# Performance work log

Measured on AMD Instinct MI355X. Metric: run time of the kernel, lower is better.

Reference implementation:

```python
import jax, jax.numpy as jnp
import numpy as np

D_MODEL = 768
N_HEADS = 8
D_K = D_MODEL // N_HEADS
D_FF = 2048
EPS = 1e-5


def _layer_norm(x, gamma, beta):
    mu = jnp.mean(x, axis=-1, keepdims=True)
    var = jnp.mean(jnp.square(x - mu), axis=-1, keepdims=True)
    return (x - mu) * jax.lax.rsqrt(var + EPS) * gamma + beta


def setup_inputs() -> dict:
    key = jax.random.key(0)
    ks = jax.random.split(key, 16)
    s = 1.0 / np.sqrt(D_MODEL)
    sf = 1.0 / np.sqrt(D_FF)
    inp = {
        "x": jax.random.normal(ks[0], (4, 2048, D_MODEL), jnp.float32),
        "Wq": jax.random.uniform(ks[1], (D_MODEL, D_MODEL), jnp.float32, -s, s),
        "bq": jnp.zeros((D_MODEL,), jnp.float32),
        "Wk": jax.random.uniform(ks[2], (D_MODEL, D_MODEL), jnp.float32, -s, s),
        "bk": jnp.zeros((D_MODEL,), jnp.float32),
        "Wv": jax.random.uniform(ks[3], (D_MODEL, D_MODEL), jnp.float32, -s, s),
        "bv": jnp.zeros((D_MODEL,), jnp.float32),
        "Wo": jax.random.uniform(ks[4], (D_MODEL, D_MODEL), jnp.float32, -s, s),
        "bo": jnp.zeros((D_MODEL,), jnp.float32),
        "g1": jnp.ones((D_MODEL,), jnp.float32),
        "be1": jnp.zeros((D_MODEL,), jnp.float32),
        "W1": jax.random.uniform(ks[5], (D_MODEL, D_FF), jnp.float32, -s, s),
        "b1": jnp.zeros((D_FF,), jnp.float32),
        "W2": jax.random.uniform(ks[6], (D_FF, D_MODEL), jnp.float32, -sf, sf),
        "b2": jnp.zeros((D_MODEL,), jnp.float32),
        "g2": jnp.ones((D_MODEL,), jnp.float32),
        "be2": jnp.zeros((D_MODEL,), jnp.float32),
    }
    return inp


def reference(x, Wq, bq, Wk, bk, Wv, bv, Wo, bo, g1, be1, W1, b1, W2, b2, g2, be2):
    B, S, D = x.shape
    residual = x
    # projections, split into heads: [B, H, S, d_k]
    def proj(W, b):
        return (x @ W + b).reshape(B, S, N_HEADS, D_K).transpose(0, 2, 1, 3)
    Q, K, V = proj(Wq, bq), proj(Wk, bk), proj(Wv, bv)
    # explicit (non-fused) attention, as in the original
    scores = jnp.einsum('bhqd,bhkd->bhqk', Q, K) / np.sqrt(D_K)  # [B,H,S,S]
    attn = jax.nn.softmax(scores, axis=-1)
    out = jnp.einsum('bhqk,bhkd->bhqd', attn, V)
    out = out.transpose(0, 2, 1, 3).reshape(B, S, D)
    out = out @ Wo + bo
    x1 = _layer_norm(residual + out, g1, be1)
    ff = jax.nn.relu(x1 @ W1 + b1) @ W2 + b2
    return _layer_norm(x1 + ff, g2, be2)
```

## Files before the change

kernel.cpp:

```cpp
#include <hip/hip_runtime.h>
#include <cstdint>
#include <cstddef>

typedef unsigned short u16;
typedef __bf16 bf16x8 __attribute__((ext_vector_type(8)));
typedef float f32x4 __attribute__((ext_vector_type(4)));
typedef float f32x16 __attribute__((ext_vector_type(16)));

#define BATCH 4
#define SEQ   2048
#define DM    768
#define NH    8
#define DK    96
#define DFF   2048
#define MTOK  8192
#define QKVN  2304
#define LOG2E 1.44269504088896340736f

__device__ __forceinline__ u16 f2bf(float f) {
  union { float f; uint32_t u; } v; v.f = f;
  return (u16)((v.u + 0x7fffu + ((v.u >> 16) & 1u)) >> 16);
}
__device__ __forceinline__ float bf2f(u16 b) {
  union { uint32_t u; float f; } v; v.u = (uint32_t)b << 16;
  return v.f;
}
__device__ __forceinline__ bf16x8 ld8(const u16* p) { return *(const bf16x8*)p; }
__device__ __forceinline__ void async16(const u16* g, u16* l) {
  __builtin_amdgcn_global_load_lds((const __attribute__((address_space(1))) void*)g,
                                   (__attribute__((address_space(3))) void*)l, 16, 0, 0);
}

__global__ __launch_bounds__(256)
void prep(const float* __restrict__ x, u16* __restrict__ xb,
          const float* __restrict__ bq, const float* __restrict__ bk,
          const float* __restrict__ bv, float* __restrict__ bqkv,
          const float* __restrict__ Wq, const float* __restrict__ Wk,
          const float* __restrict__ Wv, const float* __restrict__ Wo,
          const float* __restrict__ W1, const float* __restrict__ W2,
          u16* __restrict__ WT, u16* __restrict__ WoT,
          u16* __restrict__ W1T, u16* __restrict__ W2T) {
  __shared__ float t[32][33];
  const int tid = threadIdx.x;
  int bid = blockIdx.x;

  if (bid < 6144) {
    size_t i = (size_t)bid * 1024 + tid * 4;
    float4 f = *(const float4*)(x + i);
    uint2 o;
    o.x = (unsigned)f2bf(f.x) | ((unsigned)f2bf(f.y) << 16);
    o.y = (unsigned)f2bf(f.z) | ((unsigned)f2bf(f.w) << 16);
    *(uint2*)(xb + i) = o;
    return;
  }
  if (bid < 6153) {
    int i = (bid - 6144) * 256 + tid;
    float v = (i < 768) ? bq[i] : (i < 1536) ? bk[i - 768] : bv[i - 1536];
    bqkv[i] = v;
    return;
  }
  bid -= 6153;
  const float* in; u16* out; int C, R, bx, by;
  if (bid < 576)       { in = Wq; out = WT;                 C = 768;  R = 768;  bx = bid % 24;          by = bid / 24; }
  else if (bid < 1152) { in = Wk; out = WT + 768 * 768;     C = 768;  R = 768;  bx = (bid - 576) % 24;  by = (bid - 576) / 24; }
  else if (bid < 1728) { in = Wv; out = WT + 2 * 768 * 768; C = 768;  R = 768;  bx = (bid - 1152) % 24; by = (bid - 1152) / 24; }
  else if (bid < 2304) { in = Wo; out = WoT;                C = 768;  R = 768;  bx = (bid - 1728) % 24; by = (bid - 1728) / 24; }
  else if (bid < 3840) { in = W1; out = W1T;                C = 2048; R = 768;  bx = (bid - 2304) % 64; by = (bid - 2304) / 64; }
  else                 { in = W2; out = W2T;                C = 768;  R = 2048; bx = (bid - 3840) % 24; by = (bid - 3840) / 24; }
  const int r0 = by * 32, c0 = bx * 32;
  const int tx = tid & 31, ty = tid >> 5;
#pragma unroll
  for (int i = 0; i < 4; i++)
    t[ty + i * 8][tx] = in[(size_t)(r0 + ty + i * 8) * C + c0 + tx];
  __syncthreads();
#pragma unroll
  for (int i = 0; i < 4; i++)
    out[(size_t)(c0 + ty + i * 8) * R + r0 + tx] = f2bf(t[tx][ty + i * 8]);
}

__global__ void transpose_v(const u16* __restrict__ v, u16* __restrict__ vt) {
  __shared__ u16 t[32][33];
  int bh = blockIdx.z, b = bh >> 3, h = bh & 7;
  int s0 = blockIdx.x * 32, d0 = blockIdx.y * 32;
  int tx = threadIdx.x, ty = threadIdx.y;
#pragma unroll
  for (int i = 0; i < 4; i++)
    t[ty + i * 8][tx] = v[(size_t)(b * SEQ + s0 + ty + i * 8) * QKVN + h * DK + d0 + tx];
  __syncthreads();
#pragma unroll
  for (int i = 0; i < 4; i++)
    vt[(size_t)(bh * DK + d0 + ty + i * 8) * SEQ + s0 + tx] = t[tx][ty + i * 8];
}

template <int RESID, int RELU, int OUTBF>
__global__ __launch_bounds__(256, 4)
void gemm_bt(const u16* __restrict__ A, const u16* __restrict__ BT,
             const float* __restrict__ bias, const float* __restrict__ resid,
             float* __restrict__ Cf, u16* __restrict__ Cb, int N, int K) {
  __shared__ __align__(16) u16 lA[128 * 64];
  __shared__ __align__(16) u16 lB[128 * 64];
  const int tid = threadIdx.x;
  const int wave = tid >> 6, lane = tid & 63;
  const int quad = lane >> 4, l16 = lane & 15;
  const int wm = wave >> 1, wn = wave & 1;
  const int q8 = gridDim.x >> 3;
  const int wg = (blockIdx.x & 7) * q8 + (blockIdx.x >> 3);
  const int nbx = N >> 7;
  const int tm = (wg / nbx) * 128, tn = (wg % nbx) * 128;

  f32x4 acc[4][4] = {};

  for (int k0 = 0; k0 < K; k0 += 64) {
    __syncthreads();
#pragma unroll
    for (int i = 0; i < 4; i++) {
      int cbase = (wave * 4 + i) * 64;
      int c = cbase + lane;
      int row = c >> 3;
      int scc = (c & 7) ^ (row & 7);
      async16(A + (size_t)(tm + row) * K + k0 + scc * 8, &lA[cbase * 8]);
      async16(BT + (size_t)(tn + row) * K + k0 + scc * 8, &lB[cbase * 8]);
    }
    __syncthreads();
#pragma unroll
    for (int ks = 0; ks < 2; ks++) {
      bf16x8 af[4], bfr[4];
#pragma unroll
      for (int i = 0; i < 4; i++) {
        int ra = wm * 64 + i * 16 + l16;
        af[i] = ld8(&lA[ra * 64 + (((ks * 4 + quad) ^ (ra & 7)) << 3)]);
        int rb = wn * 64 + i * 16 + l16;
        bfr[i] = ld8(&lB[rb * 64 + (((ks * 4 + quad) ^ (rb & 7)) << 3)]);
      }
#pragma unroll
      for (int i = 0; i < 4; i++)
#pragma unroll
        for (int j = 0; j < 4; j++)
          acc[i][j] = __builtin_amdgcn_mfma_f32_16x16x32_bf16(af[i], bfr[j], acc[i][j], 0, 0, 0);
    }
  }

#pragma unroll
  for (int i = 0; i < 4; i++) {
    const int row0 = tm + wm * 64 + i * 16 + quad * 4;
#pragma unroll
    for (int j = 0; j < 4; j++) {
      const int col = tn + wn * 64 + j * 16 + l16;
      const float bv = bias[col];
#pragma unroll
      for (int r = 0; r < 4; r++) {
        float v = acc[i][j][r] + bv;
        if (RESID) v += resid[(size_t)(row0 + r) * N + col];
        if (RELU) v = fmaxf(v, 0.f);
        if (OUTBF) Cb[(size_t)(row0 + r) * N + col] = f2bf(v);
        else       Cf[(size_t)(row0 + r) * N + col] = v;
      }
    }
  }
}

template <int RESID, int RELU, int OUTBF, int RESBF>
__global__ __launch_bounds__(256, 4)
void gemm_bt64(const u16* __restrict__ A, const u16* __restrict__ BT,
               const float* __restrict__ bias, const float* __restrict__ residf,
               const u16* __restrict__ residb,
               float* __restrict__ Cf, u16* __restrict__ Cb, int N, int K) {
  __shared__ __align__(16) u16 lA[128 * 64];
  __shared__ __align__(16) u16 lB[64 * 64];
  const int tid = threadIdx.x;
  const int wave = tid >> 6, lane = tid & 63;
  const int quad = lane >> 4, l16 = lane & 15;
  const int wm = wave >> 1, wn = wave & 1;
  const int q8 = gridDim.x >> 3;
  const int wg = (blockIdx.x & 7) * q8 + (blockIdx.x >> 3);
  const int nbx = N >> 6;
  const int tm = (wg / nbx) * 128, tn = (wg % nbx) * 64;

  f32x4 acc[4][2] = {};

  for (int k0 = 0; k0 < K; k0 += 64) {
    __syncthreads();
#pragma unroll
    for (int i = 0; i < 4; i++) {
      int cbase = (wave * 4 + i) * 64;
      int c = cbase + lane;
      int row = c >> 3;
      int scc = (c & 7) ^ (row & 7);
      async16(A + (size_t)(tm + row) * K + k0 + scc * 8, &lA[cbase * 8]);
    }
#pragma unroll
    for (int i = 0; i < 2; i++) {
      int cbase = (wave * 2 + i) * 64;
      int c = cbase + lane;
      int row = c >> 3;
      int scc = (c & 7) ^ (row & 7);
      async16(BT + (size_t)(tn + row) * K + k0 + scc * 8, &lB[cbase * 8]);
    }
    __syncthreads();
#pragma unroll
    for (int ks = 0; ks < 2; ks++) {
      bf16x8 af[4], bfr[2];
#pragma unroll
      for (int i = 0; i < 4; i++) {
        int ra = wm * 64 + i * 16 + l16;
        af[i] = ld8(&lA[ra * 64 + (((ks * 4 + quad) ^ (ra & 7)) << 3)]);
      }
#pragma unroll
      for (int j = 0; j < 2; j++) {
        int rb = wn * 32 + j * 16 + l16;
        bfr[j] = ld8(&lB[rb * 64 + (((ks * 4 + quad) ^ (rb & 7)) << 3)]);
      }
#pragma unroll
      for (int i = 0; i < 4; i++)
#pragma unroll
        for (int j = 0; j < 2; j++)
          acc[i][j] = __builtin_amdgcn_mfma_f32_16x16x32_bf16(af[i], bfr[j], acc[i][j], 0, 0, 0);
    }
  }

#pragma unroll
  for (int i = 0; i < 4; i++) {
    const int row0 = tm + wm * 64 + i * 16 + quad * 4;
#pragma unroll
    for (int j = 0; j < 2; j++) {
      const int col = tn + wn * 32 + j * 16 + l16;
      const float bv = bias[col];
#pragma unroll
      for (int r = 0; r < 4; r++) {
        float v = acc[i][j][r] + bv;
        if (RESID) {
          if (RESBF) v += bf2f(residb[(size_t)(row0 + r) * N + col]);
          else       v += residf[(size_t)(row0 + r) * N + col];
        }
        if (RELU) v = fmaxf(v, 0.f);
        if (OUTBF) Cb[(size_t)(row0 + r) * N + col] = f2bf(v);
        else       Cf[(size_t)(row0 + r) * N + col] = v;
      }
    }
  }
}

#define KROW 104
#define VROW 64

#define PACK_SLICE(SC, B, DST)                                                   \
  {                                                                              \
    uint32_t u0, u1, u2, u3;                                                     \
    asm("v_cvt_pk_bf16_f32 %0, %1, %2" : "=v"(u0) : "v"(SC[B+0]), "v"(SC[B+1])); \
    asm("v_cvt_pk_bf16_f32 %0, %1, %2" : "=v"(u1) : "v"(SC[B+2]), "v"(SC[B+3])); \
    asm("v_cvt_pk_bf16_f32 %0, %1, %2" : "=v"(u2) : "v"(SC[B+4]), "v"(SC[B+5])); \
    asm("v_cvt_pk_bf16_f32 %0, %1, %2" : "=v"(u3) : "v"(SC[B+6]), "v"(SC[B+7])); \
    asm("v_permlane32_swap_b32 %0, %1" : "+v"(u2), "+v"(u0));                    \
    asm("v_permlane32_swap_b32 %0, %1" : "+v"(u3), "+v"(u1));                    \
    union { uint32_t w[4]; bf16x8 v; } pu_;                                      \
    pu_.w[0] = u0; pu_.w[1] = u1; pu_.w[2] = u2; pu_.w[3] = u3;                  \
    DST = pu_.v;                                                                 \
  }

__global__ __launch_bounds__(512, 4)
void flash_attn(const u16* __restrict__ qkv, const u16* __restrict__ Vt,
                u16* __restrict__ Ob) {
  __shared__ __align__(16) u16 smem[31744];
  const int tid = threadIdx.x, wave = tid >> 6, lane = tid & 63;
  const int l32 = lane & 31, half = lane >> 5;
  const int qsub = wave >> 1, kodd = wave & 1, pair = wave >> 1;
  const int lin = blockIdx.x;
  const int bh = (lin & 7) * 4 + ((lin >> 3) & 3);
  const int qb = lin >> 5;
  const int b = bh >> 3, h = bh & 7;
  const int q0 = qb * 128 + qsub * 32;
  const u16* Qp = qkv;
  const u16* KpB = qkv + 768 + (size_t)b * SEQ * QKVN + h * DK;
  const u16* VtB = Vt + (size_t)bh * DK * SEQ;
  const float cs = 0.10206207262f * LOG2E;
  const float Ms = 16.0f * cs;

  bf16x8 qf[6];
#pragma unroll
  for (int d = 0; d < 6; d++)
    qf[d] = ld8(Qp + (size_t)(b * SEQ + q0 + l32) * QKVN + h * DK + d * 16 + half * 8);

  f32x16 of[3] = {};
  float lp[4] = {0.f, 0.f, 0.f, 0.f};
  bf16x8 pa[2];

  auto stage = [&](int kt, int kb_, int vb_) {
    u16* kd = smem + kb_ * 6656;
    u16* vd = smem + 13312 + vb_ * 6144;
    {
      int sl = tid;
      int row = sl / 13, s = sl - row * 13;
      int c = s > 11 ? 11 : s;
      async16(KpB + (size_t)(kt + row) * QKVN + c * 8, kd + sl * 8);
    }
    if (tid < 320) {
      int sl = 512 + tid;
      int row = sl / 13, s = sl - row * 13;
      int c = s > 11 ? 11 : s;
      async16(KpB + (size_t)(kt + row) * QKVN + c * 8, kd + sl * 8);
    }
    {
      int s = tid;
      int row = s >> 3, c = (s ^ row) & 7;
      async16(VtB + (size_t)row * SEQ + kt + c * 8, vd + s * 8);
    }
    if (tid < 256) {
      int s = 512 + tid;
      int row = s >> 3, c = (s ^ row) & 7;
      async16(VtB + (size_t)row * SEQ + kt + c * 8, vd + s * 8);
    }
  };

  stage(0, 0, 0);
  int vs = 1;
  int vr = 0;
  const int krow = kodd * 32 + l32;

  for (int t = 0; t < 32; t++) {
    __syncthreads();
    if (t + 1 < 32) stage((t + 1) * 64, (t + 1) & 1, vs);
    vs = (vs == 2) ? 0 : vs + 1;

    const u16* kd = smem + (t & 1) * 6656;
    f32x16 sc = {};
    __builtin_amdgcn_s_setprio(1);
#pragma unroll
    for (int d = 0; d < 6; d++) {
      bf16x8 kb = ld8(&kd[krow * KROW + (d * 2 + half) * 8]);
      sc = __builtin_amdgcn_mfma_f32_32x32x16_bf16(kb, qf[d], sc, 0, 0, 0);
    }

    if (t > 0) {
      const u16* vd = smem + 13312 + vr * 6144;
      vr = (vr == 2) ? 0 : vr + 1;
#pragma unroll
      for (int ks = 0; ks < 2; ks++) {
        int gv = kodd * 4 + ks * 2 + half;
#pragma unroll
        for (int db = 0; db < 3; db++) {
          int vrow = db * 32 + l32;
          bf16x8 va = ld8(&vd[vrow * VROW + ((gv ^ vrow) & 7) * 8]);
          of[db] = __builtin_amdgcn_mfma_f32_32x32x16_bf16(va, pa[ks], of[db], 0, 0, 0);
        }
      }
    }
    __builtin_amdgcn_s_setprio(0);

#pragma unroll
    for (int r = 0; r < 16; r++) {
      float p = __builtin_amdgcn_exp2f(sc[r] * cs - Ms);
      lp[r & 3] += p;
      sc[r] = p;
    }
    PACK_SLICE(sc, 0, pa[0])
    PACK_SLICE(sc, 8, pa[1])
  }

  {
    const u16* vd = smem + 13312 + vr * 6144;
#pragma unroll
    for (int ks = 0; ks < 2; ks++) {
      int gv = kodd * 4 + ks * 2 + half;
#pragma unroll
      for (int db = 0; db < 3; db++) {
        int vrow = db * 32 + l32;
        bf16x8 va = ld8(&vd[vrow * VROW + ((gv ^ vrow) & 7) * 8]);
        of[db] = __builtin_amdgcn_mfma_f32_32x32x16_bf16(va, pa[ks], of[db], 0, 0, 0);
      }
    }
  }

  float l_lane = (lp[0] + lp[1]) + (lp[2] + lp[3]);
  float lw = l_lane + __shfl_xor(l_lane, 32);
  float linv = 0.f;
  float* xf = (float*)smem;
  const int q = q0 + l32;
  u16* Orow = Ob + (size_t)(b * SEQ + q) * DM + h * DK;

  __syncthreads();
  if (kodd) {
    float* dst = xf + (pair * 64 + lane) * 33;
#pragma unroll
    for (int r = 0; r < 16; r++) { dst[r] = of[0][r]; dst[16 + r] = of[1][r]; }
    dst[32] = lw;
  }
  __syncthreads();
  if (!kodd) {
    const float* src = xf + (pair * 64 + lane) * 33;
    linv = 1.f / (lw + src[32]);
#pragma unroll
    for (int db = 0; db < 2; db++)
#pragma unroll
      for (int r = 0; r < 16; r++) {
        int dk = db * 32 + (r & 3) + 8 * (r >> 2) + 4 * half;
        Orow[dk] = f2bf((of[db][r] + src[db * 16 + r]) * linv);
      }
  }
  __syncthreads();
  if (kodd) {
    float* dst = xf + (pair * 64 + lane) * 16;
#pragma unroll
    for (int r = 0; r < 16; r++) dst[r] = of[2][r];
  }
  __syncthreads();
  if (!kodd) {
    const float* src = xf + (pair * 64 + lane) * 16;
#pragma unroll
    for (int r = 0; r < 16; r++) {
      int dk = 64 + (r & 3) + 8 * (r >> 2) + 4 * half;
      Orow[dk] = f2bf((of[2][r] + src[r]) * linv);
    }
  }
}

__global__ __launch_bounds__(256)
void ln_kernel(const float* __restrict__ y, const float* __restrict__ g,
               const float* __restrict__ be, float* __restrict__ outf,
               u16* __restrict__ outb) {
  int row = blockIdx.x, t = threadIdx.x;
  const float* yr = y + (size_t)row * DM;
  float v[3], s = 0.f, s2 = 0.f;
#pragma unroll
  for (int i = 0; i < 3; i++) {
    v[i] = yr[t + i * 256];
    s += v[i];
    s2 += v[i] * v[i];
  }
#pragma unroll
  for (int m = 1; m < 64; m <<= 1) {
    s += __shfl_xor(s, m);
    s2 += __shfl_xor(s2, m);
  }
  __shared__ float red[2][4];
  int w = t >> 6;
  if ((t & 63) == 0) { red[0][w] = s; red[1][w] = s2; }
  __syncthreads();
  s = red[0][0] + red[0][1] + red[0][2] + red[0][3];
  s2 = red[1][0] + red[1][1] + red[1][2] + red[1][3];
  float mu = s * (1.f / DM);
  float var = s2 * (1.f / DM) - mu * mu;
  float rs = rsqrtf(var + 1e-5f);
#pragma unroll
  for (int i = 0; i < 3; i++) {
    int e = t + i * 256;
    float o = (v[i] - mu) * rs * g[e] + be[e];
    if (outf) outf[(size_t)row * DM + e] = o;
    if (outb) outb[(size_t)row * DM + e] = f2bf(o);
  }
}

#define SZ_BF 12582912ull
#define SZ_F  25165824ull
#define O_XB   0ull
#define O_WT   (O_XB + SZ_BF)
#define O_WOT  (O_WT + 3538944ull)
#define O_W1T  (O_WOT + 1179648ull)
#define O_W2T  (O_W1T + 3145728ull)
#define O_QKV  (O_W2T + 3145728ull)
#define O_VT   (O_QKV + 37748736ull)
#define O_Y    (O_VT + SZ_BF)
#define O_X1F  (O_Y + SZ_F)
#define O_BIAS (O_X1F + SZ_F)

extern "C" void kernel_launch(void* const* d_in, const int* in_sizes, int n_in,
                              void* d_out, int out_size, void* d_ws, size_t ws_size,
                              hipStream_t stream) {
  const float* x   = (const float*)d_in[0];
  const float* Wq  = (const float*)d_in[1];
  const float* bq  = (const float*)d_in[2];
  const float* Wk  = (const float*)d_in[3];
  const float* bk  = (const float*)d_in[4];
  const float* Wv  = (const float*)d_in[5];
  const float* bv  = (const float*)d_in[6];
  const float* Wo  = (const float*)d_in[7];
  const float* bo  = (const float*)d_in[8];
  const float* g1  = (const float*)d_in[9];
  const float* be1 = (const float*)d_in[10];
  const float* W1  = (const float*)d_in[11];
  const float* b1  = (const float*)d_in[12];
  const float* W2  = (const float*)d_in[13];
  const float* b2  = (const float*)d_in[14];
  const float* g2  = (const float*)d_in[15];
  const float* be2 = (const float*)d_in[16];
  float* out = (float*)d_out;
  char* ws = (char*)d_ws;

  u16* xb    = (u16*)(ws + O_XB);
  u16* WT    = (u16*)(ws + O_WT);
  u16* WoT   = (u16*)(ws + O_WOT);
  u16* W1T   = (u16*)(ws + O_W1T);
  u16* W2T   = (u16*)(ws + O_W2T);
  u16* qkv   = (u16*)(ws + O_QKV);
  u16* vt    = (u16*)(ws + O_VT);
  float* y   = (float*)(ws + O_Y);
  float* bqkv = (float*)(ws + O_BIAS);
  u16* ao   = xb;
  u16* x1b  = qkv;
  u16* hbuf = qkv + (size_t)MTOK * DM;

  prep<<<11529, 256, 0, stream>>>(x, xb, bq, bk, bv, bqkv,
                                  Wq, Wk, Wv, Wo, W1, W2,
                                  WT, WoT, W1T, W2T);

  gemm_bt<0, 0, 1><<<1152, 256, 0, stream>>>(xb, WT, bqkv, nullptr, nullptr, qkv, QKVN, DM);
  transpose_v<<<dim3(64, 3, 32), dim3(32, 8), 0, stream>>>(qkv + 1536, vt);
  flash_attn<<<512, 512, 0, stream>>>(qkv, vt, ao);
  gemm_bt64<1, 0, 0, 0><<<768, 256, 0, stream>>>(ao, WoT, bo, x, nullptr, y, nullptr, DM, DM);
  ln_kernel<<<8192, 256, 0, stream>>>(y, g1, be1, nullptr, x1b);
  gemm_bt<0, 1, 1><<<1024, 256, 0, stream>>>(x1b, W1T, b1, nullptr, nullptr, hbuf, DFF, DM);
  gemm_bt64<1, 0, 0, 1><<<768, 256, 0, stream>>>(hbuf, W2T, b2, nullptr, x1b, y, nullptr, DM, DFF);
  ln_kernel<<<8192, 256, 0, stream>>>(y, g2, be2, out, nullptr);
}
```

Before: 320.3 us.

## Use 256x128 tiles with 512-thread blocks for QKV and FFN1 GEMMs; double-buffer attention

The QKV and W1 GEMMs move to a new kernel with a 256-row M tile and 8 waves, which halves the block count and reuses each loaded B tile across twice as many rows. The flash-attention kernel drops its triple-buffered V staging for plain double buffering. It adds a second barrier per iteration so the next tile is issued only after the current buffers have been read. This shrinks shared memory per block and drops the min-occupancy launch bound, but the extra sync can reduce the overlap between loads and compute.

```diff
diff --git a/kernel.cpp b/kernel.cpp
--- a/kernel.cpp
+++ b/kernel.cpp
@@ -92,12 +92,12 @@
     vt[(size_t)(bh * DK + d0 + ty + i * 8) * SEQ + s0 + tx] = t[tx][ty + i * 8];
 }
 
-template <int RESID, int RELU, int OUTBF>
-__global__ __launch_bounds__(256, 4)
-void gemm_bt(const u16* __restrict__ A, const u16* __restrict__ BT,
-             const float* __restrict__ bias, const float* __restrict__ resid,
-             float* __restrict__ Cf, u16* __restrict__ Cb, int N, int K) {
-  __shared__ __align__(16) u16 lA[128 * 64];
+template <int RELU>
+__global__ __launch_bounds__(512, 4)
+void gemm_bt256(const u16* __restrict__ A, const u16* __restrict__ BT,
+                const float* __restrict__ bias,
+                u16* __restrict__ Cb, int N, int K) {
+  __shared__ __align__(16) u16 lA[256 * 64];
   __shared__ __align__(16) u16 lB[128 * 64];
   const int tid = threadIdx.x;
   const int wave = tid >> 6, lane = tid & 63;
@@ -106,7 +106,7 @@
   const int q8 = gridDim.x >> 3;
   const int wg = (blockIdx.x & 7) * q8 + (blockIdx.x >> 3);
   const int nbx = N >> 7;
-  const int tm = (wg / nbx) * 128, tn = (wg % nbx) * 128;
+  const int tm = (wg / nbx) * 256, tn = (wg % nbx) * 128;
 
   f32x4 acc[4][4] = {};
 
@@ -114,11 +114,18 @@
     __syncthreads();
 #pragma unroll
     for (int i = 0; i < 4; i++) {
-      int cbase = (wave * 4 + i) * 64;
+      int cbase = i * 512 + wave * 64;
       int c = cbase + lane;
       int row = c >> 3;
       int scc = (c & 7) ^ (row & 7);
       async16(A + (size_t)(tm + row) * K + k0 + scc * 8, &lA[cbase * 8]);
+    }
+#pragma unroll
+    for (int i = 0; i < 2; i++) {
+      int cbase = i * 512 + wave * 64;
+      int c = cbase + lane;
+      int row = c >> 3;
+      int scc = (c & 7) ^ (row & 7);
       async16(BT + (size_t)(tn + row) * K + k0 + scc * 8, &lB[cbase * 8]);
     }
     __syncthreads();
@@ -129,8 +136,11 @@
       for (int i = 0; i < 4; i++) {
         int ra = wm * 64 + i * 16 + l16;
         af[i] = ld8(&lA[ra * 64 + (((ks * 4 + quad) ^ (ra & 7)) << 3)]);
-        int rb = wn * 64 + i * 16 + l16;
-        bfr[i] = ld8(&lB[rb * 64 + (((ks * 4 + quad) ^ (rb & 7)) << 3)]);
+      }
+#pragma unroll
+      for (int j = 0; j < 4; j++) {
+        int rb = wn * 64 + j * 16 + l16;
+        bfr[j] = ld8(&lB[rb * 64 + (((ks * 4 + quad) ^ (rb & 7)) << 3)]);
       }
 #pragma unroll
       for (int i = 0; i < 4; i++)
@@ -150,10 +160,8 @@
 #pragma unroll
       for (int r = 0; r < 4; r++) {
         float v = acc[i][j][r] + bv;
-        if (RESID) v += resid[(size_t)(row0 + r) * N + col];
         if (RELU) v = fmaxf(v, 0.f);
-        if (OUTBF) Cb[(size_t)(row0 + r) * N + col] = f2bf(v);
-        else       Cf[(size_t)(row0 + r) * N + col] = v;
+        Cb[(size_t)(row0 + r) * N + col] = f2bf(v);
       }
     }
   }
@@ -257,10 +265,10 @@
     DST = pu_.v;                                                                 \
   }
 
-__global__ __launch_bounds__(512, 4)
+__global__ __launch_bounds__(512)
 void flash_attn(const u16* __restrict__ qkv, const u16* __restrict__ Vt,
                 u16* __restrict__ Ob) {
-  __shared__ __align__(16) u16 smem[31744];
+  __shared__ __align__(16) u16 smem[25600];
   const int tid = threadIdx.x, wave = tid >> 6, lane = tid & 63;
   const int l32 = lane & 31, half = lane >> 5;
   const int qsub = wave >> 1, kodd = wave & 1, pair = wave >> 1;
@@ -284,9 +292,9 @@
   float lp[4] = {0.f, 0.f, 0.f, 0.f};
   bf16x8 pa[2];
 
-  auto stage = [&](int kt, int kb_, int vb_) {
-    u16* kd = smem + kb_ * 6656;
-    u16* vd = smem + 13312 + vb_ * 6144;
+  auto stage = [&](int kt, int buf) {
+    u16* kd = smem + buf * 6656;
+    u16* vd = smem + 13312 + buf * 6144;
     {
       int sl = tid;
       int row = sl / 13, s = sl - row * 13;
@@ -311,15 +319,11 @@
     }
   };
 
-  stage(0, 0, 0);
-  int vs = 1;
-  int vr = 0;
+  stage(0, 0);
   const int krow = kodd * 32 + l32;
 
   for (int t = 0; t < 32; t++) {
     __syncthreads();
-    if (t + 1 < 32) stage((t + 1) * 64, (t + 1) & 1, vs);
-    vs = (vs == 2) ? 0 : vs + 1;
 
     const u16* kd = smem + (t & 1) * 6656;
     f32x16 sc = {};
@@ -331,8 +335,7 @@
     }
 
     if (t > 0) {
-      const u16* vd = smem + 13312 + vr * 6144;
-      vr = (vr == 2) ? 0 : vr + 1;
+      const u16* vd = smem + 13312 + ((t - 1) & 1) * 6144;
 #pragma unroll
       for (int ks = 0; ks < 2; ks++) {
         int gv = kodd * 4 + ks * 2 + half;
@@ -346,6 +349,9 @@
     }
     __builtin_amdgcn_s_setprio(0);
 
+    __syncthreads();
+    if (t + 1 < 32) stage((t + 1) * 64, (t + 1) & 1);
+
 #pragma unroll
     for (int r = 0; r < 16; r++) {
       float p = __builtin_amdgcn_exp2f(sc[r] * cs - Ms);
@@ -357,7 +363,7 @@
   }
 
   {
-    const u16* vd = smem + 13312 + vr * 6144;
+    const u16* vd = smem + 13312 + 6144;
 #pragma unroll
     for (int ks = 0; ks < 2; ks++) {
       int gv = kodd * 4 + ks * 2 + half;
@@ -502,12 +508,12 @@
                                   Wq, Wk, Wv, Wo, W1, W2,
                                   WT, WoT, W1T, W2T);
 
-  gemm_bt<0, 0, 1><<<1152, 256, 0, stream>>>(xb, WT, bqkv, nullptr, nullptr, qkv, QKVN, DM);
+  gemm_bt256<0><<<576, 512, 0, stream>>>(xb, WT, bqkv, qkv, QKVN, DM);
   transpose_v<<<dim3(64, 3, 32), dim3(32, 8), 0, stream>>>(qkv + 1536, vt);
   flash_attn<<<512, 512, 0, stream>>>(qkv, vt, ao);
   gemm_bt64<1, 0, 0, 0><<<768, 256, 0, stream>>>(ao, WoT, bo, x, nullptr, y, nullptr, DM, DM);
   ln_kernel<<<8192, 256, 0, stream>>>(y, g1, be1, nullptr, x1b);
-  gemm_bt<0, 1, 1><<<1024, 256, 0, stream>>>(x1b, W1T, b1, nullptr, nullptr, hbuf, DFF, DM);
+  gemm_bt256<1><<<512, 512, 0, stream>>>(x1b, W1T, b1, hbuf, DFF, DM);
   gemm_bt64<1, 0, 0, 1><<<768, 256, 0, stream>>>(hbuf, W2T, b2, nullptr, x1b, y, nullptr, DM, DFF);
   ln_kernel<<<8192, 256, 0, stream>>>(y, g2, be2, out, nullptr);
 }
```

New measurement: 321.9 us. About the same (+0.5%).

## Double-buffer LDS tiles in both bf16 GEMM kernels to overlap loads with MFMA

Applied to the files above, without the earlier changes.

Both GEMM kernels now use two LDS buffers per operand. The async global-to-LDS copy of the next K tile is issued right after the barrier, so it overlaps the MFMA work on the current tile instead of stalling before each compute step. This doubles LDS use per block, so the launch-bounds occupancy hints drop from 4 to 2 and 3 blocks, which costs some latency hiding from concurrent workgroups.

```diff
diff --git a/kernel.cpp b/kernel.cpp
--- a/kernel.cpp
+++ b/kernel.cpp
@@ -93,12 +93,12 @@
 }
 
 template <int RESID, int RELU, int OUTBF>
-__global__ __launch_bounds__(256, 4)
+__global__ __launch_bounds__(256, 2)
 void gemm_bt(const u16* __restrict__ A, const u16* __restrict__ BT,
              const float* __restrict__ bias, const float* __restrict__ resid,
              float* __restrict__ Cf, u16* __restrict__ Cb, int N, int K) {
-  __shared__ __align__(16) u16 lA[128 * 64];
-  __shared__ __align__(16) u16 lB[128 * 64];
+  __shared__ __align__(16) u16 lA[2][128 * 64];
+  __shared__ __align__(16) u16 lB[2][128 * 64];
   const int tid = threadIdx.x;
   const int wave = tid >> 6, lane = tid & 63;
   const int quad = lane >> 4, l16 = lane & 15;
@@ -110,27 +110,33 @@
 
   f32x4 acc[4][4] = {};
 
-  for (int k0 = 0; k0 < K; k0 += 64) {
-    __syncthreads();
+  auto stage = [&](int buf, int k0) {
 #pragma unroll
     for (int i = 0; i < 4; i++) {
       int cbase = (wave * 4 + i) * 64;
       int c = cbase + lane;
       int row = c >> 3;
       int scc = (c & 7) ^ (row & 7);
-      async16(A + (size_t)(tm + row) * K + k0 + scc * 8, &lA[cbase * 8]);
-      async16(BT + (size_t)(tn + row) * K + k0 + scc * 8, &lB[cbase * 8]);
-    }
+      async16(A + (size_t)(tm + row) * K + k0 + scc * 8, &lA[buf][cbase * 8]);
+      async16(BT + (size_t)(tn + row) * K + k0 + scc * 8, &lB[buf][cbase * 8]);
+    }
+  };
+
+  const int NK = K >> 6;
+  stage(0, 0);
+  for (int it = 0; it < NK; ++it) {
+    const int cur = it & 1;
     __syncthreads();
+    if (it + 1 < NK) stage(cur ^ 1, (it + 1) << 6);
 #pragma unroll
     for (int ks = 0; ks < 2; ks++) {
       bf16x8 af[4], bfr[4];
 #pragma unroll
       for (int i = 0; i < 4; i++) {
         int ra = wm * 64 + i * 16 + l16;
-        af[i] = ld8(&lA[ra * 64 + (((ks * 4 + quad) ^ (ra & 7)) << 3)]);
+        af[i] = ld8(&lA[cur][ra * 64 + (((ks * 4 + quad) ^ (ra & 7)) << 3)]);
         int rb = wn * 64 + i * 16 + l16;
-        bfr[i] = ld8(&lB[rb * 64 + (((ks * 4 + quad) ^ (rb & 7)) << 3)]);
+        bfr[i] = ld8(&lB[cur][rb * 64 + (((ks * 4 + quad) ^ (rb & 7)) << 3)]);
       }
 #pragma unroll
       for (int i = 0; i < 4; i++)
@@ -160,13 +166,13 @@
 }
 
 template <int RESID, int RELU, int OUTBF, int RESBF>
-__global__ __launch_bounds__(256, 4)
+__global__ __launch_bounds__(256, 3)
 void gemm_bt64(const u16* __restrict__ A, const u16* __restrict__ BT,
                const float* __restrict__ bias, const float* __restrict__ residf,
                const u16* __restrict__ residb,
                float* __restrict__ Cf, u16* __restrict__ Cb, int N, int K) {
-  __shared__ __align__(16) u16 lA[128 * 64];
-  __shared__ __align__(16) u16 lB[64 * 64];
+  __shared__ __align__(16) u16 lA[2][128 * 64];
+  __shared__ __align__(16) u16 lB[2][64 * 64];
   const int tid = threadIdx.x;
   const int wave = tid >> 6, lane = tid & 63;
   const int quad = lane >> 4, l16 = lane & 15;
@@ -178,15 +184,14 @@
 
   f32x4 acc[4][2] = {};
 
-  for (int k0 = 0; k0 < K; k0 += 64) {
-    __syncthreads();
+  auto stage = [&](int buf, int k0) {
 #pragma unroll
     for (int i = 0; i < 4; i++) {
       int cbase = (wave * 4 + i) * 64;
       int c = cbase + lane;
       int row = c >> 3;
       int scc = (c & 7) ^ (row & 7);
-      async16(A + (size_t)(tm + row) * K + k0 + scc * 8, &lA[cbase * 8]);
+      async16(A + (size_t)(tm + row) * K + k0 + scc * 8, &lA[buf][cbase * 8]);
     }
 #pragma unroll
     for (int i = 0; i < 2; i++) {
@@ -194,21 +199,28 @@
       int c = cbase + lane;
       int row = c >> 3;
       int scc = (c & 7) ^ (row & 7);
-      async16(BT + (size_t)(tn + row) * K + k0 + scc * 8, &lB[cbase * 8]);
-    }
+      async16(BT + (size_t)(tn + row) * K + k0 + scc * 8, &lB[buf][cbase * 8]);
+    }
+  };
+
+  const int NK = K >> 6;
+  stage(0, 0);
+  for (int it = 0; it < NK; ++it) {
+    const int cur = it & 1;
     __syncthreads();
+    if (it + 1 < NK) stage(cur ^ 1, (it + 1) << 6);
 #pragma unroll
     for (int ks = 0; ks < 2; ks++) {
       bf16x8 af[4], bfr[2];
 #pragma unroll
       for (int i = 0; i < 4; i++) {
         int ra = wm * 64 + i * 16 + l16;
-        af[i] = ld8(&lA[ra * 64 + (((ks * 4 + quad) ^ (ra & 7)) << 3)]);
+        af[i] = ld8(&lA[cur][ra * 64 + (((ks * 4 + quad) ^ (ra & 7)) << 3)]);
       }
 #pragma unroll
       for (int j = 0; j < 2; j++) {
         int rb = wn * 32 + j * 16 + l16;
-        bfr[j] = ld8(&lB[rb * 64 + (((ks * 4 + quad) ^ (rb & 7)) << 3)]);
+        bfr[j] = ld8(&lB[cur][rb * 64 + (((ks * 4 + quad) ^ (rb & 7)) << 3)]);
       }
 #pragma unroll
       for (int i = 0; i < 4; i++)
```

Result: slower. 330.2 us (+3.1%).

## Replace QKV and FFN1 GEMMs with 256x256 double-buffered 8-wave pipelined kernel

Applied to the files above, without the earlier changes.

The 128x128 single-buffered GEMM used for the QKV projection and the first FFN layer is replaced by a 512-thread kernel with 256x256 tiles. It double-buffers LDS, prefetching the next K-slice asynchronously in halves between MFMA phases, and raises wave priority with s_setprio around the MFMA bursts. The aim is to hide global-load latency behind compute and raise data reuse per tile. The cost is 128 KB of LDS per block and fewer blocks (288 and 256), which lowers occupancy and can leave CUs idle on the tail wave.

```diff
diff --git a/kernel.cpp b/kernel.cpp
--- a/kernel.cpp
+++ b/kernel.cpp
@@ -92,57 +92,126 @@
     vt[(size_t)(bh * DK + d0 + ty + i * 8) * SEQ + s0 + tx] = t[tx][ty + i * 8];
 }
 
-template <int RESID, int RELU, int OUTBF>
-__global__ __launch_bounds__(256, 4)
-void gemm_bt(const u16* __restrict__ A, const u16* __restrict__ BT,
-             const float* __restrict__ bias, const float* __restrict__ resid,
-             float* __restrict__ Cf, u16* __restrict__ Cb, int N, int K) {
-  __shared__ __align__(16) u16 lA[128 * 64];
-  __shared__ __align__(16) u16 lB[128 * 64];
+template <int RELU>
+__global__ __launch_bounds__(512, 2)
+void gemm8p(const u16* __restrict__ A, const u16* __restrict__ BT,
+            const float* __restrict__ bias, u16* __restrict__ Cb,
+            int N, int K) {
+  __shared__ __align__(16) u16 lA[2][256 * 64];
+  __shared__ __align__(16) u16 lB[2][256 * 64];
   const int tid = threadIdx.x;
   const int wave = tid >> 6, lane = tid & 63;
   const int quad = lane >> 4, l16 = lane & 15;
-  const int wm = wave >> 1, wn = wave & 1;
+  const int wm = wave >> 2, wn = wave & 3;
   const int q8 = gridDim.x >> 3;
   const int wg = (blockIdx.x & 7) * q8 + (blockIdx.x >> 3);
-  const int nbx = N >> 7;
-  const int tm = (wg / nbx) * 128, tn = (wg % nbx) * 128;
-
-  f32x4 acc[4][4] = {};
-
-  for (int k0 = 0; k0 < K; k0 += 64) {
+  const int nbx = N >> 8;
+  const int tm = (wg / nbx) * 256, tn = (wg % nbx) * 256;
+  const u16* Ab = A + (size_t)tm * K;
+  const u16* Bb = BT + (size_t)tn * K;
+
+  f32x4 acc[8][4] = {};
+
+  auto stageH = [&](const u16* src, u16* dstbuf, int k0, int base) {
+#pragma unroll
+    for (int i = 0; i < 2; i++) {
+      int g = base + i * 512 + tid;
+      int row = g >> 3;
+      int sc = (g & 7) ^ (row & 7);
+      async16(src + (size_t)row * K + k0 + sc * 8,
+              dstbuf + (base + i * 512 + wave * 64) * 8);
+    }
+  };
+
+  const int NK = K >> 6;
+  stageH(Ab, lA[0], 0, 0);  stageH(Ab, lA[0], 0, 1024);
+  stageH(Bb, lB[0], 0, 0);  stageH(Bb, lB[0], 0, 1024);
+
+  for (int it = 0; it < NK; ++it) {
+    const int cur = it & 1;
+    const int k0n = (it + 1) << 6;
+    const bool pf = (it + 1 < NK);
     __syncthreads();
+    const u16* la = lA[cur];
+    const u16* lb = lB[cur];
+    bf16x8 bf[4], af[4];
+
+#pragma unroll
+    for (int j = 0; j < 4; j++) {
+      int rb = wn * 64 + j * 16 + l16;
+      bf[j] = ld8(&lb[rb * 64 + ((quad ^ (rb & 7)) << 3)]);
+    }
 #pragma unroll
     for (int i = 0; i < 4; i++) {
-      int cbase = (wave * 4 + i) * 64;
-      int c = cbase + lane;
-      int row = c >> 3;
-      int scc = (c & 7) ^ (row & 7);
-      async16(A + (size_t)(tm + row) * K + k0 + scc * 8, &lA[cbase * 8]);
-      async16(BT + (size_t)(tn + row) * K + k0 + scc * 8, &lB[cbase * 8]);
-    }
-    __syncthreads();
-#pragma unroll
-    for (int ks = 0; ks < 2; ks++) {
-      bf16x8 af[4], bfr[4];
-#pragma unroll
-      for (int i = 0; i < 4; i++) {
-        int ra = wm * 64 + i * 16 + l16;
-        af[i] = ld8(&lA[ra * 64 + (((ks * 4 + quad) ^ (ra & 7)) << 3)]);
-        int rb = wn * 64 + i * 16 + l16;
-        bfr[i] = ld8(&lB[rb * 64 + (((ks * 4 + quad) ^ (rb & 7)) << 3)]);
-      }
-#pragma unroll
-      for (int i = 0; i < 4; i++)
-#pragma unroll
-        for (int j = 0; j < 4; j++)
-          acc[i][j] = __builtin_amdgcn_mfma_f32_16x16x32_bf16(af[i], bfr[j], acc[i][j], 0, 0, 0);
-    }
-  }
-
-#pragma unroll
-  for (int i = 0; i < 4; i++) {
-    const int row0 = tm + wm * 64 + i * 16 + quad * 4;
+      int ra = wm * 128 + i * 16 + l16;
+      af[i] = ld8(&la[ra * 64 + ((quad ^ (ra & 7)) << 3)]);
+    }
+    if (pf) { stageH(Ab, lA[cur ^ 1], k0n, 0); stageH(Bb, lB[cur ^ 1], k0n, 0); }
+    __builtin_amdgcn_s_barrier();
+    __builtin_amdgcn_s_setprio(1);
+#pragma unroll
+    for (int i = 0; i < 4; i++)
+#pragma unroll
+      for (int j = 0; j < 4; j++)
+        acc[i][j] = __builtin_amdgcn_mfma_f32_16x16x32_bf16(af[i], bf[j], acc[i][j], 0, 0, 0);
+    __builtin_amdgcn_s_setprio(0);
+    __builtin_amdgcn_s_barrier();
+
+#pragma unroll
+    for (int i = 0; i < 4; i++) {
+      int ra = wm * 128 + (i + 4) * 16 + l16;
+      af[i] = ld8(&la[ra * 64 + ((quad ^ (ra & 7)) << 3)]);
+    }
+    if (pf) { stageH(Ab, lA[cur ^ 1], k0n, 1024); stageH(Bb, lB[cur ^ 1], k0n, 1024); }
+    __builtin_amdgcn_s_barrier();
+    __builtin_amdgcn_s_setprio(1);
+#pragma unroll
+    for (int i = 0; i < 4; i++)
+#pragma unroll
+      for (int j = 0; j < 4; j++)
+        acc[i + 4][j] = __builtin_amdgcn_mfma_f32_16x16x32_bf16(af[i], bf[j], acc[i + 4][j], 0, 0, 0);
+    __builtin_amdgcn_s_setprio(0);
+    __builtin_amdgcn_s_barrier();
+
+#pragma unroll
+    for (int j = 0; j < 4; j++) {
+      int rb = wn * 64 + j * 16 + l16;
+      bf[j] = ld8(&lb[rb * 64 + (((4 + quad) ^ (rb & 7)) << 3)]);
+    }
+#pragma unroll
+    for (int i = 0; i < 4; i++) {
+      int ra = wm * 128 + i * 16 + l16;
+      af[i] = ld8(&la[ra * 64 + (((4 + quad) ^ (ra & 7)) << 3)]);
+    }
+    __builtin_amdgcn_s_barrier();
+    __builtin_amdgcn_s_setprio(1);
+#pragma unroll
+    for (int i = 0; i < 4; i++)
+#pragma unroll
+      for (int j = 0; j < 4; j++)
+        acc[i][j] = __builtin_amdgcn_mfma_f32_16x16x32_bf16(af[i], bf[j], acc[i][j], 0, 0, 0);
+    __builtin_amdgcn_s_setprio(0);
+    __builtin_amdgcn_s_barrier();
+
+#pragma unroll
+    for (int i = 0; i < 4; i++) {
+      int ra = wm * 128 + (i + 4) * 16 + l16;
+      af[i] = ld8(&la[ra * 64 + (((4 + quad) ^ (ra & 7)) << 3)]);
+    }
+    __builtin_amdgcn_s_barrier();
+    __builtin_amdgcn_s_setprio(1);
+#pragma unroll
+    for (int i = 0; i < 4; i++)
+#pragma unroll
+      for (int j = 0; j < 4; j++)
+        acc[i + 4][j] = __builtin_amdgcn_mfma_f32_16x16x32_bf16(af[i], bf[j], acc[i + 4][j], 0, 0, 0);
+    __builtin_amdgcn_s_setprio(0);
+    __builtin_amdgcn_s_barrier();
+  }
+
+#pragma unroll
+  for (int i = 0; i < 8; i++) {
+    const int row0 = tm + wm * 128 + i * 16 + quad * 4;
 #pragma unroll
     for (int j = 0; j < 4; j++) {
       const int col = tn + wn * 64 + j * 16 + l16;
@@ -150,10 +219,8 @@
 #pragma unroll
       for (int r = 0; r < 4; r++) {
         float v = acc[i][j][r] + bv;
-        if (RESID) v += resid[(size_t)(row0 + r) * N + col];
         if (RELU) v = fmaxf(v, 0.f);
-        if (OUTBF) Cb[(size_t)(row0 + r) * N + col] = f2bf(v);
-        else       Cf[(size_t)(row0 + r) * N + col] = v;
+        Cb[(size_t)(row0 + r) * N + col] = f2bf(v);
       }
     }
   }
@@ -502,12 +569,12 @@
                                   Wq, Wk, Wv, Wo, W1, W2,
                                   WT, WoT, W1T, W2T);
 
-  gemm_bt<0, 0, 1><<<1152, 256, 0, stream>>>(xb, WT, bqkv, nullptr, nullptr, qkv, QKVN, DM);
+  gemm8p<0><<<288, 512, 0, stream>>>(xb, WT, bqkv, qkv, QKVN, DM);
   transpose_v<<<dim3(64, 3, 32), dim3(32, 8), 0, stream>>>(qkv + 1536, vt);
   flash_attn<<<512, 512, 0, stream>>>(qkv, vt, ao);
   gemm_bt64<1, 0, 0, 0><<<768, 256, 0, stream>>>(ao, WoT, bo, x, nullptr, y, nullptr, DM, DM);
   ln_kernel<<<8192, 256, 0, stream>>>(y, g1, be1, nullptr, x1b);
-  gemm_bt<0, 1, 1><<<1024, 256, 0, stream>>>(x1b, W1T, b1, nullptr, nullptr, hbuf, DFF, DM);
+  gemm8p<1><<<256, 512, 0, stream>>>(x1b, W1T, b1, hbuf, DFF, DM);
   gemm_bt64<1, 0, 0, 1><<<768, 256, 0, stream>>>(hbuf, W2T, b2, nullptr, x1b, y, nullptr, DM, DFF);
   ln_kernel<<<8192, 256, 0, stream>>>(y, g2, be2, out, nullptr);
 }
```

Measured after the change: 336.6 us. 1.05x slower.
